# Kernel optimization log

Measured on AMD Instinct MI355X. Metric: run time of the kernel, lower is better.

Reference implementation:

```python
import jax, jax.numpy as jnp
import numpy as np

K_CAND = 64
K_FINAL = 16
ALPHA = 0.5
CURV_RATIO = 0.5
EPS = 1e-8


def index_points(points, idx):
    # points: [B, N, C], idx: [B, ...] -> [B, ..., C]
    B, N, C = points.shape
    flat = idx.reshape(B, -1)
    g = jnp.take_along_axis(points, flat[..., None], axis=1)
    return g.reshape(idx.shape + (C,))


def fps(points, num_fps):
    # Furthest point sampling (matches pointnet2: starts from index 0).
    B, N, _ = points.shape
    barange = jnp.arange(B)

    def body(carry, _):
        mindist, last_idx = carry
        last_pt = points[barange, last_idx]                       # [B, 3]
        d = jnp.sum((points - last_pt[:, None, :]) ** 2, axis=-1)  # [B, N]
        mindist = jnp.minimum(mindist, d)
        next_idx = jnp.argmax(mindist, axis=1).astype(jnp.int32)
        return (mindist, next_idx), last_idx

    init = (jnp.full((B, N), 1e10, points.dtype), jnp.zeros((B,), jnp.int32))
    _, idxs = jax.lax.scan(body, init, None, length=num_fps)
    return idxs.T  # [B, num_fps]


def znorm(x):
    # per-cloud normalization over points dim, unbiased std like torch
    return (x - x.mean(axis=1, keepdims=True)) / (x.std(axis=1, ddof=1, keepdims=True) + EPS)


def reference(xyz, features, w1, b1, w2, b2, num_samples):
    B, N, _ = xyz.shape
    # --- candidate kNN via pairwise squared distances (same ordering as cdist) ---
    sq = jnp.sum(xyz * xyz, axis=-1)                               # [B, N]
    d2 = sq[:, :, None] + sq[:, None, :] - 2.0 * jnp.einsum('bnc,bmc->bnm', xyz, xyz)
    _, cand = jax.lax.top_k(-d2, K_CAND + 1)                       # smallest dists first
    cand = cand[:, :, 1:]                                          # drop self -> [B, N, 64]

    # --- learned neighbor scoring MLP on relative geometry/features ---
    nxyz = index_points(xyz, cand)                                 # [B, N, 64, 3]
    nfeat = index_points(features, cand)                           # [B, N, 64, C]
    rel_xyz = nxyz - xyz[:, :, None, :]
    rel_feat = nfeat - features[:, :, None, :]
    mlp_in = jnp.concatenate([rel_xyz, rel_feat], axis=-1)         # [B, N, 64, 3+C]
    h = jax.nn.gelu(mlp_in @ w1 + b1, approximate=False)
    scores = (h @ w2 + b2)[..., 0]                                 # [B, N, 64]
    _, top_in_cand = jax.lax.top_k(scores, K_FINAL)
    final_idx = jnp.take_along_axis(cand, top_in_cand, axis=2)     # [B, N, 16]

    # --- robust importance: curvature (3x3 SVD of cov) + feature variation ---
    n2xyz = index_points(xyz, final_idx)                           # [B, N, 16, 3]
    n2feat = index_points(features, final_idx)
    dxyz = n2xyz - xyz[:, :, None, :]
    cov = jnp.einsum('bnki,bnkj->bnij', dxyz, dxyz) / K_FINAL      # [B, N, 3, 3]
    s = jnp.linalg.svd(cov, compute_uv=False)                      # descending, [B, N, 3]
    l2, l1, l0 = s[..., 0] ** 2, s[..., 1] ** 2, s[..., 2] ** 2
    curvature = l0 / (l0 + l1 + l2 + EPS)
    dfeat = n2feat - features[:, :, None, :]
    feat_var = jnp.linalg.norm(dfeat, axis=-1).mean(axis=-1)       # [B, N]
    importance = znorm(curvature) + ALPHA * znorm(feat_var)

    # --- select curvature points, mask them, FPS for the rest ---
    num_curv = int(num_samples * CURV_RATIO)
    num_fps = num_samples - num_curv
    _, curv_idx = jax.lax.top_k(importance, num_curv)              # [B, num_curv]
    far_val = jnp.max(xyz) + 1.0
    barange = jnp.arange(B)[:, None]
    masked_xyz = xyz.at[barange, curv_idx].set(far_val)
    fps_idx = fps(masked_xyz, num_fps).astype(curv_idx.dtype)      # [B, num_fps]
    merged = jnp.concatenate([curv_idx, fps_idx], axis=1)          # [B, num_samples]
    sampled_xyz = index_points(xyz, merged)                        # [B, num_samples, 3]
    return sampled_xyz, merged


def setup_inputs() -> dict:
    key = jax.random.key(0)
    k1, k2, k3, k4 = jax.random.split(key, 4)
    B, N, C = 2, 8192, 64
    xyz = jax.random.normal(k1, (B, N, 3), jnp.float32)
    features = jax.random.normal(k2, (B, N, C), jnp.float32)
    fan_in1 = 3 + C
    w1 = jax.random.normal(k3, (fan_in1, 128), jnp.float32) / np.sqrt(fan_in1)
    b1 = jnp.zeros((128,), jnp.float32)
    w2 = jax.random.normal(k4, (128, 1), jnp.float32) / np.sqrt(128)
    b2 = jnp.zeros((1,), jnp.float32)
    return {"xyz": xyz, "features": features, "w1": w1, "b1": b1,
            "w2": w2, "b2": b2, "num_samples": 2048}
```

## Files before the change

### kernel.cpp

```cpp
#include <hip/hip_runtime.h>
#include <hip/hip_bf16.h>
#include <math.h>

#define N 8192
#define BATCH 2
#define NROWS (BATCH*N)

typedef float v2f __attribute__((ext_vector_type(2)));

static __device__ __forceinline__ float fsubr(float a, float b){ return __fadd_rn(a, -b); }
static __device__ __forceinline__ unsigned okey(float f){
  unsigned u = __float_as_uint(f);
  return (u & 0x80000000u) ? ~u : (u | 0x80000000u);
}

__global__ void aux_kernel(const float* __restrict__ xyz, float* __restrict__ xs, float* __restrict__ ys,
                           float* __restrict__ zs, float* __restrict__ sq, float4* __restrict__ mxyz){
  int i = blockIdx.x*256 + threadIdx.x;
  if (i < NROWS){
    float x = xyz[i*3+0], y = xyz[i*3+1], z = xyz[i*3+2];
    xs[i]=x; ys[i]=y; zs[i]=z;
    sq[i] = __fadd_rn(__fadd_rn(__fmul_rn(x,x),__fmul_rn(y,y)),__fmul_rn(z,z));
    mxyz[i] = make_float4(x, y, z, 0.0f);
  }
}

__global__ void farval_kernel(const float* __restrict__ xyz, float* __restrict__ farval){
  __shared__ float lm[4];
  float m = -1e30f;
  for (int i = threadIdx.x; i < NROWS*3; i += 256) m = fmaxf(m, xyz[i]);
  for (int off = 32; off; off >>= 1) m = fmaxf(m, __shfl_down(m, off));
  if ((threadIdx.x & 63) == 0) lm[threadIdx.x >> 6] = m;
  __syncthreads();
  if (threadIdx.x == 0){
    float r = fmaxf(fmaxf(lm[0],lm[1]), fmaxf(lm[2],lm[3]));
    farval[0] = __fadd_rn(r, 1.0f);
  }
}

__global__ __launch_bounds__(128) void q_kernel(const float* __restrict__ xyz, const float* __restrict__ feat,
                                                const float* __restrict__ w1, float* __restrict__ Q){
  __shared__ float sx[16][3];
  __shared__ float sf[16][64];
  const int t = threadIdx.x;
  const int row0 = blockIdx.x * 16;
  for (int j = t; j < 1024; j += 128) sf[j>>6][j&63] = feat[(size_t)row0*64 + j];
  if (t < 48) sx[t/3][t%3] = xyz[(size_t)row0*3 + t];
  __syncthreads();
  float acc[16];
  #pragma unroll
  for (int r = 0; r < 16; ++r) acc[r] = 0.0f;
  for (int c = 0; c < 3; ++c){
    float wv = w1[c*128 + t];
    #pragma unroll
    for (int r = 0; r < 16; ++r) acc[r] = fmaf(sx[r][c], wv, acc[r]);
  }
  for (int c = 0; c < 64; ++c){
    float wv = w1[(3+c)*128 + t];
    #pragma unroll
    for (int r = 0; r < 16; ++r) acc[r] = fmaf(sf[r][c], wv, acc[r]);
  }
  #pragma unroll
  for (int r = 0; r < 16; ++r) Q[(size_t)(row0+r)*128 + t] = acc[r];
}

#define BINBASE 0xBA00
__global__ __launch_bounds__(512) void knn_kernel(const float* __restrict__ xs, const float* __restrict__ ys,
                                                  const float* __restrict__ zs, const float* __restrict__ sq,
                                                  int* __restrict__ cand){
#pragma clang fp contract(off)
  __shared__ unsigned fk[N];
  __shared__ unsigned hist[2048];
  __shared__ unsigned long long win[1024];
  __shared__ int scal[8];
  const int t = threadIdx.x;
  const int base_row = blockIdx.x * 32;
  const int b = base_row >> 13;
  const int n0 = base_row & (N-1);
  const int pbase = b * N;
  v2f px[8], py[8], pz[8], ps[8];
  #pragma unroll
  for (int k = 0; k < 8; ++k){
    int i0 = t + (2*k)*512, i1 = t + (2*k+1)*512;
    px[k].x = xs[pbase+i0]; px[k].y = xs[pbase+i1];
    py[k].x = ys[pbase+i0]; py[k].y = ys[pbase+i1];
    pz[k].x = zs[pbase+i0]; pz[k].y = zs[pbase+i1];
    ps[k].x = sq[pbase+i0]; ps[k].y = sq[pbase+i1];
  }
  for (int r = 0; r < 32; ++r){
    const int n = n0 + r;
    const float qx = xs[pbase+n], qy = ys[pbase+n], qz = zs[pbase+n], qs = sq[pbase+n];
    #pragma unroll
    for (int j = 0; j < 4; ++j) hist[t + j*512] = 0;
    __syncthreads();
    #pragma unroll
    for (int k = 0; k < 8; ++k){
      v2f dot = px[k]*qx + py[k]*qy + pz[k]*qz;
      v2f dd  = (qs + ps[k]) - 2.0f*dot;
      unsigned u0 = okey(dd.x), u1 = okey(dd.y);
      fk[t + (2*k)*512] = u0;
      fk[t + (2*k+1)*512] = u1;
      int bin0 = (int)(u0 >> 16) - BINBASE; bin0 = bin0 < 0 ? 0 : (bin0 > 2047 ? 2047 : bin0);
      int bin1 = (int)(u1 >> 16) - BINBASE; bin1 = bin1 < 0 ? 0 : (bin1 > 2047 ? 2047 : bin1);
      atomicAdd(&hist[bin0], 1u);
      atomicAdd(&hist[bin1], 1u);
    }
    __syncthreads();
    if (t < 64){
      unsigned s = 0;
      for (int k2 = 0; k2 < 32; ++k2) s += hist[t*32 + ((k2 + t) & 31)];
      unsigned p = s;
      for (int off = 1; off < 64; off <<= 1){ unsigned v = (unsigned)__shfl_up((int)p, off); if (t >= off) p += v; }
      int excl = (int)(p - s);
      if (excl < 65 && (int)p >= 65){ scal[0] = t; scal[1] = excl; }
    }
    __syncthreads();
    {
      int g = scal[0];
      if (t < 32){
        unsigned s = hist[g*32 + t];
        unsigned p = s;
        for (int off = 1; off < 32; off <<= 1){ unsigned v = (unsigned)__shfl_up((int)p, off); if (t >= off) p += v; }
        int before = scal[1] + (int)(p - s);
        if (before < 65 && scal[1] + (int)p >= 65) scal[2] = g*32 + t;
      }
    }
    if (t == 0) scal[3] = 0;
    __syncthreads();
    int B1 = scal[2];
    unsigned limit = (B1 >= 2047) ? 0xFFFFFFFFu : ((unsigned)(BINBASE + B1 + 1) << 16);
    #pragma unroll
    for (int j = 0; j < 16; ++j){
      int i = t + j*512;
      unsigned u = fk[i];
      if (u < limit){
        int p = atomicAdd(&scal[3], 1);
        if (p < 1024) win[p] = ((unsigned long long)u << 32) | (unsigned)i;
      }
    }
    __syncthreads();
    int m = scal[3]; if (m > 1024) m = 1024;
    for (int e = t; e < m; e += 512){
      unsigned long long me = win[e];
      int rk = 0;
      for (int j2 = 0; j2 < m; ++j2) rk += (win[j2] < me) ? 1 : 0;
      if (rk >= 1 && rk < 65) cand[(size_t)(pbase + n)*64 + (rk-1)] = (int)(me & 0xFFFFFFFFull);
    }
    __syncthreads();
  }
}

__global__ __launch_bounds__(256) void score_kernel(const float* __restrict__ xyz, const float* __restrict__ feat,
                                                    const float* __restrict__ Q, const float* __restrict__ b1,
                                                    const float* __restrict__ w2, const float* __restrict__ b2,
                                                    const int* __restrict__ cand,
                                                    float* __restrict__ curv, float* __restrict__ fv){
  __shared__ float4 sb14[32], sw24[32];
  __shared__ int ssel[4][16];
  __shared__ float sdx[4][16], sdy[4][16], sdz[4][16], snrm[4][16];
  const int t = threadIdx.x;
  if (t < 32) sb14[t] = ((const float4*)b1)[t];
  else if (t < 64) sw24[t-32] = ((const float4*)w2)[t-32];
  __syncthreads();
  const int w = t >> 6, lane = t & 63;
  const int row = blockIdx.x*4 + w;
  const int b = row >> 13;
  const int pbase = b * N;
  const int n = row & (N-1);
  const int ck = cand[(size_t)row*64 + lane];
  const float4* Qn4 = (const float4*)(Q + (size_t)row * 128);
  const float4* Qc4 = (const float4*)(Q + (size_t)(pbase + ck) * 128);
  const float ks = 0.70710678118654752440f;
  float acc = 0.0f;
  for (int c = 0; c < 32; ++c){
    float4 qc = Qc4[c], qn = Qn4[c], bb = sb14[c], ww = sw24[c];
    float p0 = (qc.x - qn.x) + bb.x;
    float g0 = 0.5f * p0 * (1.0f + erff(p0 * ks));
    acc += g0 * ww.x;
    float p1 = (qc.y - qn.y) + bb.y;
    float g1 = 0.5f * p1 * (1.0f + erff(p1 * ks));
    acc += g1 * ww.y;
    float p2 = (qc.z - qn.z) + bb.z;
    float g2 = 0.5f * p2 * (1.0f + erff(p2 * ks));
    acc += g2 * ww.z;
    float p3 = (qc.w - qn.w) + bb.w;
    float g3 = 0.5f * p3 * (1.0f + erff(p3 * ks));
    acc += g3 * ww.w;
  }
  float score = acc + b2[0];
  unsigned key = okey(score);
  int rk = 0;
  for (int j = 0; j < 64; ++j){
    unsigned kj = (unsigned)__shfl((int)key, j);
    rk += (kj > key || (kj == key && j < lane)) ? 1 : 0;
  }
  float cx = xyz[(size_t)(pbase+ck)*3+0], cy = xyz[(size_t)(pbase+ck)*3+1], cz = xyz[(size_t)(pbase+ck)*3+2];
  float qxv = xyz[(size_t)(pbase+n)*3+0], qyv = xyz[(size_t)(pbase+n)*3+1], qzv = xyz[(size_t)(pbase+n)*3+2];
  if (rk < 16){
    ssel[w][rk] = ck;
    sdx[w][rk] = fsubr(cx, qxv);
    sdy[w][rk] = fsubr(cy, qyv);
    sdz[w][rk] = fsubr(cz, qzv);
  }
  __syncthreads();
  if (lane < 16){
    int si = ssel[w][lane];
    const float4* fc4 = (const float4*)(feat + (size_t)(pbase+si)*64);
    const float4* fn4 = (const float4*)(feat + (size_t)(pbase+n)*64);
    double s = 0.0;
    for (int c = 0; c < 16; ++c){
      float4 a = fc4[c], bq = fn4[c];
      float d0 = fsubr(a.x, bq.x); s += (double)d0 * (double)d0;
      float d1 = fsubr(a.y, bq.y); s += (double)d1 * (double)d1;
      float d2 = fsubr(a.z, bq.z); s += (double)d2 * (double)d2;
      float d3 = fsubr(a.w, bq.w); s += (double)d3 * (double)d3;
    }
    snrm[w][lane] = sqrtf((float)s);
  }
  __syncthreads();
  if (lane == 0){
    double cxx=0, cxy=0, cxz=0, cyy=0, cyz=0, czz=0;
    for (int k2 = 0; k2 < 16; ++k2){
      double dx = (double)sdx[w][k2], dy = (double)sdy[w][k2], dz = (double)sdz[w][k2];
      cxx += dx*dx; cxy += dx*dy; cxz += dx*dz; cyy += dy*dy; cyz += dy*dz; czz += dz*dz;
    }
    float fxx = (float)(cxx/16.0), fxy = (float)(cxy/16.0), fxz = (float)(cxz/16.0);
    float fyy = (float)(cyy/16.0), fyz = (float)(cyz/16.0), fzz = (float)(czz/16.0);
    double a = fxx, bbv = fyy, c = fzz, d = fxy, e = fyz, f = fxz;
    double p1 = d*d + f*f + e*e;
    double e0, e1, e2v;
    if (p1 == 0.0){ e0 = a; e1 = bbv; e2v = c; }
    else {
      double q = (a + bbv + c) / 3.0;
      double aa = a - q, bq = bbv - q, cc = c - q;
      double p2 = aa*aa + bq*bq + cc*cc + 2.0*p1;
      double p = sqrt(p2 / 6.0);
      double inv = 1.0 / p;
      double bxx = aa*inv, byy = bq*inv, bzz = cc*inv, bxy = d*inv, bxz = f*inv, byz = e*inv;
      double detB = bxx*(byy*bzz - byz*byz) - bxy*(bxy*bzz - byz*bxz) + bxz*(bxy*byz - byy*bxz);
      double rr = 0.5 * detB;
      rr = fmin(1.0, fmax(-1.0, rr));
      double phi = acos(rr) / 3.0;
      e0 = q + 2.0*p*cos(phi);
      e2v = q + 2.0*p*cos(phi + 2.0943951023931953);
      e1 = 3.0*q - e0 - e2v;
    }
    double s0 = fabs(e0), s1 = fabs(e1), s2d = fabs(e2v), tt;
    if (s0 < s1){ tt=s0; s0=s1; s1=tt; }
    if (s1 < s2d){ tt=s1; s1=s2d; s2d=tt; }
    if (s0 < s1){ tt=s0; s0=s1; s1=tt; }
    float sv0 = (float)s0, sv1 = (float)s1, sv2 = (float)s2d;
    float l2f = __fmul_rn(sv0,sv0), l1f = __fmul_rn(sv1,sv1), l0f = __fmul_rn(sv2,sv2);
    float den = __fadd_rn(__fadd_rn(__fadd_rn(l0f, l1f), l2f), 1e-8f);
    curv[row] = l0f / den;
    double fs = 0.0;
    for (int k2 = 0; k2 < 16; ++k2) fs += (double)snrm[w][k2];
    fv[row] = (float)(fs / 16.0);
  }
}

static __device__ __forceinline__ double blk_sum(double v, double* lds, int t){
  for (int off = 32; off; off >>= 1) v += __shfl_down(v, off);
  int w = t >> 6, lane = t & 63;
  if (lane == 0) lds[w] = v;
  __syncthreads();
  double r = (t < 16) ? lds[t] : 0.0;
  if (t < 64){ for (int off = 8; off; off >>= 1) r += __shfl_down(r, off); }
  if (t == 0) lds[0] = r;
  __syncthreads();
  double out = lds[0];
  __syncthreads();
  return out;
}

__global__ __launch_bounds__(1024) void stats_kernel(const float* __restrict__ curv, const float* __restrict__ fv,
                                                     float* __restrict__ imp){
  __shared__ double lds[16];
  const int t = threadIdx.x;
  const int base = blockIdx.x * N;
  double sc = 0, sf = 0;
  for (int j = 0; j < 8; ++j){ int i = t + j*1024; sc += (double)curv[base+i]; sf += (double)fv[base+i]; }
  double Sc = blk_sum(sc, lds, t);
  double Sf = blk_sum(sf, lds, t);
  double mc = Sc/8192.0, mf = Sf/8192.0;
  double vc = 0, vf = 0;
  for (int j = 0; j < 8; ++j){ int i = t + j*1024;
    double d1 = (double)curv[base+i] - mc; vc += d1*d1;
    double d2 = (double)fv[base+i]  - mf; vf += d2*d2; }
  double Vc = blk_sum(vc, lds, t);
  double Vf = blk_sum(vf, lds, t);
  float mcf = (float)mc, mff = (float)mf;
  float dc = __fadd_rn((float)sqrt(Vc/8191.0), 1e-8f);
  float df = __fadd_rn((float)sqrt(Vf/8191.0), 1e-8f);
  for (int j = 0; j < 8; ++j){ int i = t + j*1024;
    float zc = fsubr(curv[base+i], mcf) / dc;
    float zf = fsubr(fv[base+i],  mff) / df;
    imp[base+i] = __fadd_rn(zc, __fmul_rn(0.5f, zf));
  }
}

__global__ __launch_bounds__(1024) void topk_kernel(const float* __restrict__ imp, int* __restrict__ merged,
                                                    float4* __restrict__ mxyz, const float* __restrict__ farval){
  __shared__ unsigned dk[N];
  __shared__ unsigned hist[2048];
  __shared__ unsigned long long win[2048];
  __shared__ int scal[8];
  const int t = threadIdx.x;
  const int b = blockIdx.x;
  const int base = b * N;
  #pragma unroll
  for (int j = 0; j < 2; ++j) hist[t + j*1024] = 0;
  if (t == 0) scal[3] = 0;
  __syncthreads();
  for (int j = 0; j < 8; ++j){
    int i = t + j*1024;
    unsigned u = ~okey(imp[base+i]);
    dk[i] = u;
    atomicAdd(&hist[u >> 21], 1u);
  }
  __syncthreads();
  if (t < 64){
    unsigned s = 0;
    for (int k2 = 0; k2 < 32; ++k2) s += hist[t*32 + ((k2 + t) & 31)];
    unsigned p = s;
    for (int off = 1; off < 64; off <<= 1){ unsigned v = (unsigned)__shfl_up((int)p, off); if (t >= off) p += v; }
    int excl = (int)(p - s);
    if (excl < 1024 && (int)p >= 1024){ scal[0] = t; scal[1] = excl; }
  }
  __syncthreads();
  {
    int g = scal[0];
    if (t < 32){
      unsigned s = hist[g*32 + t];
      unsigned p = s;
      for (int off = 1; off < 32; off <<= 1){ unsigned v = (unsigned)__shfl_up((int)p, off); if (t >= off) p += v; }
      int before = scal[1] + (int)(p - s);
      if (before < 1024 && scal[1] + (int)p >= 1024) scal[2] = g*32 + t;
    }
  }
  __syncthreads();
  unsigned B1 = (unsigned)scal[2];
  unsigned limit = (B1 >= 2047u) ? 0xFFFFFFFFu : ((B1+1u) << 21);
  for (int j = 0; j < 8; ++j){
    int i = t + j*1024;
    unsigned u = dk[i];
    if (u < limit){
      int p = atomicAdd(&scal[3], 1);
      if (p < 2048) win[p] = ((unsigned long long)u << 13) | (unsigned)i;
    }
  }
  __syncthreads();
  int m = scal[3]; if (m > 2048) m = 2048;
  const float far = farval[0];
  for (int e = t; e < m; e += 1024){
    unsigned long long me = win[e];
    int rk = 0;
    for (int j2 = 0; j2 < m; ++j2) rk += (win[j2] < me) ? 1 : 0;
    if (rk < 1024){
      int idx = (int)(me & 0x1FFFull);
      merged[b*2048 + rk] = idx;
      mxyz[base + idx] = make_float4(far, far, far, 0.0f);
    }
  }
}

#define FPS_LOAD(k) { int i0=t+(2*k)*512, i1=t+(2*k+1)*512; \
    float4 a0 = mxyz[base+i0], a1 = mxyz[base+i1]; stab[i0]=a0; stab[i1]=a1; \
    px##k=(v2f){a0.x,a1.x}; py##k=(v2f){a0.y,a1.y}; pz##k=(v2f){a0.z,a1.z}; md##k=(v2f){1e10f,1e10f}; }
#define FPS_UPD(k) { v2f dx=px##k-lx, dy=py##k-ly, dz=pz##k-lz; \
    v2f d=dx*dx+dy*dy+dz*dz; md##k=__builtin_elementwise_min(md##k,d); \
    vmax=__builtin_elementwise_max(vmax,md##k); }
#define FPS_PICK(k) { if (md##k.y == wmf) blow = 8191u - (unsigned)(t + ((2*k+1)<<9)); \
    if (md##k.x == wmf) blow = 8191u - (unsigned)(t + ((2*k)<<9)); }
#define DPPMAXF(CTRL) { int mo = __builtin_amdgcn_update_dpp(0, __float_as_int(wm), (CTRL), 0xf, 0xf, true); \
    wm = fmaxf(wm, __int_as_float(mo)); }
#define DPPMAXU(CTRL) { int mo = __builtin_amdgcn_update_dpp(0, (int)blow, (CTRL), 0xf, 0xf, true); \
    blow = (blow > (unsigned)mo) ? blow : (unsigned)mo; }

__global__ __launch_bounds__(512, 1) void fps_kernel(const float4* __restrict__ mxyz, int* __restrict__ merged){
#pragma clang fp contract(off)
  extern __shared__ float4 stab[];
  __shared__ unsigned long long wkey[2][8];
  const int t = threadIdx.x;
  const int b = blockIdx.x;
  const int base = b * N;
  v2f px0,px1,px2,px3,px4,px5,px6,px7;
  v2f py0,py1,py2,py3,py4,py5,py6,py7;
  v2f pz0,pz1,pz2,pz3,pz4,pz5,pz6,pz7;
  v2f md0,md1,md2,md3,md4,md5,md6,md7;
  FPS_LOAD(0) FPS_LOAD(1) FPS_LOAD(2) FPS_LOAD(3)
  FPS_LOAD(4) FPS_LOAD(5) FPS_LOAD(6) FPS_LOAD(7)
  if (t == 0) merged[b*2048 + 1024] = 0;
  __syncthreads();
  float4 w0 = stab[0];
  float lx = w0.x, ly = w0.y, lz = w0.z;
  for (int it = 0; it < 1023; ++it){
    v2f vmax; vmax.x = -1.0f; vmax.y = -1.0f;
    FPS_UPD(0) FPS_UPD(1) FPS_UPD(2) FPS_UPD(3)
    FPS_UPD(4) FPS_UPD(5) FPS_UPD(6) FPS_UPD(7)
    float wm = fmaxf(vmax.x, vmax.y);
    DPPMAXF(0x111) DPPMAXF(0x112) DPPMAXF(0x114) DPPMAXF(0x118)
    DPPMAXF(0x142) DPPMAXF(0x143)
    const float wmf = __int_as_float(__builtin_amdgcn_readlane(__float_as_int(wm), 63));
    unsigned blow = 0u;
    FPS_PICK(7) FPS_PICK(6) FPS_PICK(5) FPS_PICK(4)
    FPS_PICK(3) FPS_PICK(2) FPS_PICK(1) FPS_PICK(0)
    DPPMAXU(0x111) DPPMAXU(0x112) DPPMAXU(0x114) DPPMAXU(0x118)
    DPPMAXU(0x142) DPPMAXU(0x143)
    if ((t & 63) == 63)
      wkey[it & 1][t >> 6] = ((unsigned long long)__float_as_uint(wmf) << 13) | (unsigned long long)blow;
    __syncthreads();
    const unsigned long long* wk = wkey[it & 1];
    unsigned long long k = wk[0];
    #pragma unroll
    for (int i2 = 1; i2 < 8; ++i2){ unsigned long long o = wk[i2]; if (o > k) k = o; }
    const int idx = 8191 - (int)(k & 0x1FFFull);
    if (t == 0) merged[b*2048 + 1024 + it + 1] = idx;
    float4 wv = stab[idx];
    lx = wv.x; ly = wv.y; lz = wv.z;
  }
}

__global__ void finalize_kernel(const float* __restrict__ xyz, const int* __restrict__ merged,
                                float* __restrict__ out){
  int i = blockIdx.x*256 + threadIdx.x;
  if (i < BATCH*2048){
    int b = i >> 11;
    int idx = merged[i];
    out[12288 + i] = (float)idx;
    const float* p = xyz + (size_t)(b*N + idx)*3;
    out[i*3+0] = p[0]; out[i*3+1] = p[1]; out[i*3+2] = p[2];
  }
}

extern "C" void kernel_launch(void* const* d_in, const int* in_sizes, int n_in,
                              void* d_out, int out_size, void* d_ws, size_t ws_size,
                              hipStream_t stream){
  const float* xyz  = (const float*)d_in[0];
  const float* feat = (const float*)d_in[1];
  const float* w1   = (const float*)d_in[2];
  const float* b1   = (const float*)d_in[3];
  const float* w2   = (const float*)d_in[4];
  const float* b2   = (const float*)d_in[5];
  float* out = (float*)d_out;
  char* ws = (char*)d_ws;
  float*  Q      = (float*) (ws);
  int*    cand   = (int*)   (ws + 8388608);
  float*  xs     = (float*) (ws + 12582912);
  float*  ysv    = (float*) (ws + 12648448);
  float*  zsv    = (float*) (ws + 12713984);
  float*  sq     = (float*) (ws + 12779520);
  float*  curv   = (float*) (ws + 12845056);
  float*  fv     = (float*) (ws + 12910592);
  float*  imp    = (float*) (ws + 12976128);
  int*    merged = (int*)   (ws + 13041664);
  float*  farval = (float*) (ws + 13058048);
  float4* mxyz   = (float4*)(ws + 13058112);

  aux_kernel<<<64, 256, 0, stream>>>(xyz, xs, ysv, zsv, sq, mxyz);
  farval_kernel<<<1, 256, 0, stream>>>(xyz, farval);
  q_kernel<<<1024, 128, 0, stream>>>(xyz, feat, w1, Q);
  knn_kernel<<<512, 512, 0, stream>>>(xs, ysv, zsv, sq, cand);
  score_kernel<<<4096, 256, 0, stream>>>(xyz, feat, Q, b1, w2, b2, cand, curv, fv);
  stats_kernel<<<2, 1024, 0, stream>>>(curv, fv, imp);
  topk_kernel<<<2, 1024, 0, stream>>>(imp, merged, mxyz, farval);
  fps_kernel<<<2, 512, 131072, stream>>>(mxyz, merged);
  finalize_kernel<<<16, 256, 0, stream>>>(xyz, merged, out);
}
```

Baseline: 1.647 ms.

## Morton-sort points per thread and skip FPS updates for distant thread clusters

Adds a sort kernel that bins each cloud's points into a 16^3 Morton grid, so each FPS thread owns 16 spatially contiguous points. Each thread keeps a bounding sphere and skips the distance update when the last selected point is provably too far to lower its min distances. It reuses its cached best key instead, cutting FPS ALU work on the serial 1023-iteration loop. This costs an extra kernel launch, wider keys that carry both sorted and original indices, and a possible tie-breaking or rounding-margin mismatch with the reference.

Result: slower. 1.888 ms (+14.6%).

```diff
diff --git a/kernel.cpp b/kernel.cpp
--- a/kernel.cpp
+++ b/kernel.cpp
@@ -12,6 +12,9 @@
 static __device__ __forceinline__ unsigned okey(float f){
   unsigned u = __float_as_uint(f);
   return (u & 0x80000000u) ? ~u : (u | 0x80000000u);
+}
+static __device__ __forceinline__ unsigned spread3(unsigned v){
+  return (v & 1u) | ((v & 2u) << 2) | ((v & 4u) << 4) | ((v & 8u) << 6);
 }
 
 __global__ void aux_kernel(const float* __restrict__ xyz, float* __restrict__ xs, float* __restrict__ ys,
@@ -364,20 +367,104 @@
   }
 }
 
-#define FPS_LOAD(k) { int i0=t+(2*k)*512, i1=t+(2*k+1)*512; \
-    float4 a0 = mxyz[base+i0], a1 = mxyz[base+i1]; stab[i0]=a0; stab[i1]=a1; \
-    px##k=(v2f){a0.x,a1.x}; py##k=(v2f){a0.y,a1.y}; pz##k=(v2f){a0.z,a1.z}; md##k=(v2f){1e10f,1e10f}; }
+__global__ __launch_bounds__(1024) void sort_kernel(const float4* __restrict__ mxyz, float4* __restrict__ psort){
+  __shared__ unsigned hist[4096];
+  __shared__ float r6[16][6];
+  __shared__ float bounds[6];
+  __shared__ unsigned wsum[16];
+  const int t = threadIdx.x;
+  const int b = blockIdx.x;
+  const int base = b * N;
+  const int lane = t & 63, wv = t >> 6;
+  float4 p[8];
+  #pragma unroll
+  for (int j = 0; j < 8; ++j) p[j] = mxyz[base + t + j*1024];
+  float mnx=p[0].x, mxx=p[0].x, mny=p[0].y, mxy=p[0].y, mnz=p[0].z, mxz=p[0].z;
+  #pragma unroll
+  for (int j = 1; j < 8; ++j){
+    mnx=fminf(mnx,p[j].x); mxx=fmaxf(mxx,p[j].x);
+    mny=fminf(mny,p[j].y); mxy=fmaxf(mxy,p[j].y);
+    mnz=fminf(mnz,p[j].z); mxz=fmaxf(mxz,p[j].z);
+  }
+  #pragma unroll
+  for (int off = 32; off; off >>= 1){
+    mnx=fminf(mnx,__shfl_down(mnx,off)); mxx=fmaxf(mxx,__shfl_down(mxx,off));
+    mny=fminf(mny,__shfl_down(mny,off)); mxy=fmaxf(mxy,__shfl_down(mxy,off));
+    mnz=fminf(mnz,__shfl_down(mnz,off)); mxz=fmaxf(mxz,__shfl_down(mxz,off));
+  }
+  if (lane == 0){ r6[wv][0]=mnx; r6[wv][1]=mxx; r6[wv][2]=mny; r6[wv][3]=mxy; r6[wv][4]=mnz; r6[wv][5]=mxz; }
+  #pragma unroll
+  for (int j = 0; j < 4; ++j) hist[t + j*1024] = 0;
+  __syncthreads();
+  if (t == 0){
+    float a0=r6[0][0], a1=r6[0][1], a2=r6[0][2], a3=r6[0][3], a4=r6[0][4], a5=r6[0][5];
+    for (int i = 1; i < 16; ++i){
+      a0=fminf(a0,r6[i][0]); a1=fmaxf(a1,r6[i][1]);
+      a2=fminf(a2,r6[i][2]); a3=fmaxf(a3,r6[i][3]);
+      a4=fminf(a4,r6[i][4]); a5=fmaxf(a5,r6[i][5]);
+    }
+    bounds[0]=a0; bounds[1]=a1; bounds[2]=a2; bounds[3]=a3; bounds[4]=a4; bounds[5]=a5;
+  }
+  __syncthreads();
+  const float bx0=bounds[0], by0=bounds[2], bz0=bounds[4];
+  const float sxm = 16.0f / fmaxf(bounds[1]-bx0, 1e-9f);
+  const float sym = 16.0f / fmaxf(bounds[3]-by0, 1e-9f);
+  const float szm = 16.0f / fmaxf(bounds[5]-bz0, 1e-9f);
+  unsigned keys[8];
+  #pragma unroll
+  for (int j = 0; j < 8; ++j){
+    int cx = (int)((p[j].x - bx0)*sxm); cx = cx<0?0:(cx>15?15:cx);
+    int cy = (int)((p[j].y - by0)*sym); cy = cy<0?0:(cy>15?15:cy);
+    int cz = (int)((p[j].z - bz0)*szm); cz = cz<0?0:(cz>15?15:cz);
+    unsigned k = (spread3((unsigned)cx)<<2) | (spread3((unsigned)cy)<<1) | spread3((unsigned)cz);
+    keys[j] = k;
+    atomicAdd(&hist[k], 1u);
+  }
+  __syncthreads();
+  unsigned h0=hist[t*4+0], h1=hist[t*4+1], h2=hist[t*4+2], h3=hist[t*4+3];
+  unsigned s = h0+h1+h2+h3;
+  unsigned pr = s;
+  #pragma unroll
+  for (int off = 1; off < 64; off <<= 1){ unsigned v = (unsigned)__shfl_up((int)pr, off); if (lane >= off) pr += v; }
+  if (lane == 63) wsum[wv] = pr;
+  __syncthreads();
+  if (t == 0){ unsigned run = 0; for (int i = 0; i < 16; ++i){ unsigned tmp = wsum[i]; wsum[i] = run; run += tmp; } }
+  __syncthreads();
+  unsigned excl = pr - s + wsum[wv];
+  __syncthreads();
+  hist[t*4+0]=excl; excl+=h0; hist[t*4+1]=excl; excl+=h1; hist[t*4+2]=excl; excl+=h2; hist[t*4+3]=excl;
+  __syncthreads();
+  #pragma unroll
+  for (int j = 0; j < 8; ++j){
+    unsigned pos = atomicAdd(&hist[keys[j]], 1u);
+    psort[base + pos] = make_float4(p[j].x, p[j].y, p[j].z, __uint_as_float((unsigned)(t + j*1024)));
+  }
+}
+
+#define RED8(op, a) op(op(op(a##0,a##1),op(a##2,a##3)),op(op(a##4,a##5),op(a##6,a##7)))
+#define FPS_LOAD(k) { \
+    int i0 = t*16 + 2*(k), i1 = i0 + 1; \
+    float4 a0 = psort[base + i0], a1 = psort[base + i1]; \
+    stab[i0] = a0; stab[i1] = a1; \
+    px##k=(v2f){a0.x,a1.x}; py##k=(v2f){a0.y,a1.y}; pz##k=(v2f){a0.z,a1.z}; \
+    md##k=(v2f){1e10f,1e10f}; \
+    lo##k##a = ((8191u - __float_as_uint(a0.w)) << 13) | (unsigned)i0; \
+    lo##k##b = ((8191u - __float_as_uint(a1.w)) << 13) | (unsigned)i1; }
 #define FPS_UPD(k) { v2f dx=px##k-lx, dy=py##k-ly, dz=pz##k-lz; \
-    v2f d=dx*dx+dy*dy+dz*dz; md##k=__builtin_elementwise_min(md##k,d); \
-    vmax=__builtin_elementwise_max(vmax,md##k); }
-#define FPS_PICK(k) { if (md##k.y == wmf) blow = 8191u - (unsigned)(t + ((2*k+1)<<9)); \
-    if (md##k.x == wmf) blow = 8191u - (unsigned)(t + ((2*k)<<9)); }
+    v2f d=dx*dx+dy*dy+dz*dz; md##k=__builtin_elementwise_min(md##k,d); }
+#define FPS_PICK(k) { \
+    if (md##k.x == wmf && lo##k##a > blow) blow = lo##k##a; \
+    if (md##k.y == wmf && lo##k##b > blow) blow = lo##k##b; }
+#define R2M(k) { v2f dx=px##k-ccx, dy=py##k-ccy, dz=pz##k-ccz; \
+    v2f r2=dx*dx+dy*dy+dz*dz; r2m=fmaxf(r2m,fmaxf(r2.x,r2.y)); }
 #define DPPMAXF(CTRL) { int mo = __builtin_amdgcn_update_dpp(0, __float_as_int(wm), (CTRL), 0xf, 0xf, true); \
     wm = fmaxf(wm, __int_as_float(mo)); }
 #define DPPMAXU(CTRL) { int mo = __builtin_amdgcn_update_dpp(0, (int)blow, (CTRL), 0xf, 0xf, true); \
     blow = (blow > (unsigned)mo) ? blow : (unsigned)mo; }
 
-__global__ __launch_bounds__(512, 1) void fps_kernel(const float4* __restrict__ mxyz, int* __restrict__ merged){
+__global__ __launch_bounds__(512, 1) void fps_kernel(const float4* __restrict__ psort,
+                                                     const float4* __restrict__ mxyz,
+                                                     int* __restrict__ merged){
 #pragma clang fp contract(off)
   extern __shared__ float4 stab[];
   __shared__ unsigned long long wkey[2][8];
@@ -388,35 +475,60 @@
   v2f py0,py1,py2,py3,py4,py5,py6,py7;
   v2f pz0,pz1,pz2,pz3,pz4,pz5,pz6,pz7;
   v2f md0,md1,md2,md3,md4,md5,md6,md7;
+  unsigned lo0a,lo0b,lo1a,lo1b,lo2a,lo2b,lo3a,lo3b,lo4a,lo4b,lo5a,lo5b,lo6a,lo6b,lo7a,lo7b;
   FPS_LOAD(0) FPS_LOAD(1) FPS_LOAD(2) FPS_LOAD(3)
   FPS_LOAD(4) FPS_LOAD(5) FPS_LOAD(6) FPS_LOAD(7)
+  v2f mn2 = RED8(__builtin_elementwise_min, px);
+  v2f mx2 = RED8(__builtin_elementwise_max, px);
+  const float ccx = 0.5f*(fminf(mn2.x,mn2.y) + fmaxf(mx2.x,mx2.y));
+  mn2 = RED8(__builtin_elementwise_min, py);
+  mx2 = RED8(__builtin_elementwise_max, py);
+  const float ccy = 0.5f*(fminf(mn2.x,mn2.y) + fmaxf(mx2.x,mx2.y));
+  mn2 = RED8(__builtin_elementwise_min, pz);
+  mx2 = RED8(__builtin_elementwise_max, pz);
+  const float ccz = 0.5f*(fminf(mn2.x,mn2.y) + fmaxf(mx2.x,mx2.y));
+  float r2m = 0.0f;
+  R2M(0) R2M(1) R2M(2) R2M(3) R2M(4) R2M(5) R2M(6) R2M(7)
+  const float rr = sqrtf(r2m) * 1.00001f + 1e-9f;
+  float rad2 = 3e38f;
+  unsigned long long ckey = 0ull;
   if (t == 0) merged[b*2048 + 1024] = 0;
   __syncthreads();
-  float4 w0 = stab[0];
+  float4 w0 = mxyz[base];
   float lx = w0.x, ly = w0.y, lz = w0.z;
   for (int it = 0; it < 1023; ++it){
-    v2f vmax; vmax.x = -1.0f; vmax.y = -1.0f;
-    FPS_UPD(0) FPS_UPD(1) FPS_UPD(2) FPS_UPD(3)
-    FPS_UPD(4) FPS_UPD(5) FPS_UPD(6) FPS_UPD(7)
-    float wm = fmaxf(vmax.x, vmax.y);
-    DPPMAXF(0x111) DPPMAXF(0x112) DPPMAXF(0x114) DPPMAXF(0x118)
-    DPPMAXF(0x142) DPPMAXF(0x143)
-    const float wmf = __int_as_float(__builtin_amdgcn_readlane(__float_as_int(wm), 63));
-    unsigned blow = 0u;
-    FPS_PICK(7) FPS_PICK(6) FPS_PICK(5) FPS_PICK(4)
-    FPS_PICK(3) FPS_PICK(2) FPS_PICK(1) FPS_PICK(0)
-    DPPMAXU(0x111) DPPMAXU(0x112) DPPMAXU(0x114) DPPMAXU(0x118)
-    DPPMAXU(0x142) DPPMAXU(0x143)
-    if ((t & 63) == 63)
-      wkey[it & 1][t >> 6] = ((unsigned long long)__float_as_uint(wmf) << 13) | (unsigned long long)blow;
+    float dxc = ccx-lx, dyc = ccy-ly, dzc = ccz-lz;
+    float dc2 = dxc*dxc + dyc*dyc + dzc*dzc;
+    bool active = !(dc2 * 0.99999f > rad2);
+    if (__ballot(active)){
+      FPS_UPD(0) FPS_UPD(1) FPS_UPD(2) FPS_UPD(3)
+      FPS_UPD(4) FPS_UPD(5) FPS_UPD(6) FPS_UPD(7)
+      v2f vm2 = RED8(__builtin_elementwise_max, md);
+      const float bestv = fmaxf(vm2.x, vm2.y);
+      float wm = bestv;
+      DPPMAXF(0x111) DPPMAXF(0x112) DPPMAXF(0x114) DPPMAXF(0x118)
+      DPPMAXF(0x142) DPPMAXF(0x143)
+      const float wmf = __int_as_float(__builtin_amdgcn_readlane(__float_as_int(wm), 63));
+      unsigned blow = 0u;
+      FPS_PICK(0) FPS_PICK(1) FPS_PICK(2) FPS_PICK(3)
+      FPS_PICK(4) FPS_PICK(5) FPS_PICK(6) FPS_PICK(7)
+      DPPMAXU(0x111) DPPMAXU(0x112) DPPMAXU(0x114) DPPMAXU(0x118)
+      DPPMAXU(0x142) DPPMAXU(0x143)
+      if ((t & 63) == 63)
+        ckey = ((unsigned long long)__float_as_uint(wmf) << 26) | (unsigned long long)blow;
+      const float rad = rr + sqrtf(bestv) * 1.00001f + 1e-9f;
+      rad2 = rad * rad * 1.00001f + 1e-9f;
+    }
+    if ((t & 63) == 63) wkey[it & 1][t >> 6] = ckey;
     __syncthreads();
     const unsigned long long* wk = wkey[it & 1];
     unsigned long long k = wk[0];
     #pragma unroll
     for (int i2 = 1; i2 < 8; ++i2){ unsigned long long o = wk[i2]; if (o > k) k = o; }
-    const int idx = 8191 - (int)(k & 0x1FFFull);
-    if (t == 0) merged[b*2048 + 1024 + it + 1] = idx;
-    float4 wv = stab[idx];
+    const int spos = (int)(k & 0x1FFFull);
+    const int orig = 8191 - (int)((k >> 13) & 0x1FFFull);
+    if (t == 0) merged[b*2048 + 1024 + it + 1] = orig;
+    float4 wv = stab[spos];
     lx = wv.x; ly = wv.y; lz = wv.z;
   }
 }
@@ -456,6 +568,7 @@
   int*    merged = (int*)   (ws + 13041664);
   float*  farval = (float*) (ws + 13058048);
   float4* mxyz   = (float4*)(ws + 13058112);
+  float4* psort  = (float4*)(ws + 13320256);
 
   aux_kernel<<<64, 256, 0, stream>>>(xyz, xs, ysv, zsv, sq, mxyz);
   farval_kernel<<<1, 256, 0, stream>>>(xyz, farval);
@@ -464,6 +577,7 @@
   score_kernel<<<4096, 256, 0, stream>>>(xyz, feat, Q, b1, w2, b2, cand, curv, fv);
   stats_kernel<<<2, 1024, 0, stream>>>(curv, fv, imp);
   topk_kernel<<<2, 1024, 0, stream>>>(imp, merged, mxyz, farval);
-  fps_kernel<<<2, 512, 131072, stream>>>(mxyz, merged);
+  sort_kernel<<<2, 1024, 0, stream>>>(mxyz, psort);
+  fps_kernel<<<2, 512, 131072, stream>>>(psort, mxyz, merged);
   finalize_kernel<<<16, 256, 0, stream>>>(xyz, merged, out);
 }
```
